# Kernel optimization log

Hardware: AMD Instinct MI355X
Metric: run time of the kernel (lower is better)

Reference implementation:

```python
import jax, jax.numpy as jnp
import numpy as np

TEMP = 0.05  # contrastive temperature (ContrastiveLoss.temp)
N, D = 8192, 128


def setup_inputs() -> dict:
    key = jax.random.key(0)
    k1, k2 = jax.random.split(key)
    x = jax.random.normal(k1, (N, D), dtype=jnp.float32)
    # Binary positive-pair label matrix; diagonal forced to 1 so every row
    # has at least one positive (positive_pair_nums > 0).
    y = (jax.random.uniform(k2, (N, N)) < 0.05).astype(jnp.float32)
    y = jnp.maximum(y, jnp.eye(N, dtype=jnp.float32))
    return {"x": x, "y": y}


def reference(x, y):
    # similarity(): L2-normalize rows, cosine matmul, exp(cos / temp)
    x_norm = x / jnp.linalg.norm(x, axis=1, keepdims=True)        # [N, D]
    cos_sim = jnp.exp(jnp.matmul(x_norm, x_norm.T) / TEMP)        # [N, N]

    positive_pair_nums = jnp.sum(y, axis=-1)                      # [N]
    neg_y = 1.0 - y
    # hard_mode == 'normal': negative mass per anchor
    nl = jnp.sum(cos_sim * neg_y, axis=-1, keepdims=True)         # [N, 1]

    # sm = log(cos_sim / (cos_sim + nl)); average over positives per row
    sm = jnp.log(cos_sim / (cos_sim + nl))                        # [N, N]
    lm = jnp.sum(sm * y, axis=-1) / positive_pair_nums            # [N]
    return -jnp.mean(lm)
```

## Files before the change

kernel.cpp:

```cpp
#include <hip/hip_runtime.h>
#include <hip/hip_bf16.h>


#define NN 8192

typedef short bf16x8 __attribute__((ext_vector_type(8)));
typedef float f32x4 __attribute__((ext_vector_type(4)));
typedef unsigned long long u64;
typedef unsigned int u32;

__device__ inline unsigned short f32_to_bf16_rne(float f) {
    unsigned u = __float_as_uint(f);
    unsigned r = 0x7FFFu + ((u >> 16) & 1u);
    return (unsigned short)((u + r) >> 16);
}

__global__ __launch_bounds__(256) void prep_kernel(
    const float* __restrict__ x, const float* __restrict__ y,
    unsigned short* __restrict__ xn, u64* __restrict__ bits) {
    const int t = threadIdx.x;
    const int w = t >> 6, l = t & 63;
    if (blockIdx.x < 2048) {
        const int row = blockIdx.x * 4 + w;
        float2 v = reinterpret_cast<const float2*>(x)[row * 64 + l];
        float ss = v.x * v.x + v.y * v.y;
#pragma unroll
        for (int m = 1; m < 64; m <<= 1) ss += __shfl_xor(ss, m);
        float rn = 1.0f / sqrtf(ss);
        ushort2 st;
        st.x = f32_to_bf16_rne(v.x * rn);
        st.y = f32_to_bf16_rne(v.y * rn);
        reinterpret_cast<ushort2*>(xn)[row * 64 + l] = st;
    } else {
        const int gw = (blockIdx.x - 2048) * 4 + w;
#pragma unroll 1
        for (int it = 0; it < 32; ++it) {
            const size_t w0 = ((size_t)it * 8192 + gw) * 4;
            u64 m0 = __ballot(y[(w0 + 0) * 64 + l] != 0.0f);
            u64 m1 = __ballot(y[(w0 + 1) * 64 + l] != 0.0f);
            u64 m2 = __ballot(y[(w0 + 2) * 64 + l] != 0.0f);
            u64 m3 = __ballot(y[(w0 + 3) * 64 + l] != 0.0f);
            if (l == 0) {
                bits[w0 + 0] = m0;
                bits[w0 + 1] = m1;
                bits[w0 + 2] = m2;
                bits[w0 + 3] = m3;
            }
        }
    }
}

template <bool DIAG>
__device__ __forceinline__ void epilogue(
    const f32x4 (&acc)[4][4], const u64 (&bw)[4], int l, int lm16, int lh4,
    int wM, int wN, int R0, int cb, float* __restrict__ Pt,
    float* __restrict__ sdg) {
#pragma unroll
    for (int qq = 0; qq < 4; ++qq) {
        float T = 0.0f, A = 0.0f, Y = 0.0f;
        const u32 lo = (u32)bw[qq];
        const u32 hi = (u32)(bw[qq] >> 32);
        const int rl = qq * 16 + lm16;
#pragma unroll
        for (int p = 0; p < 4; ++p) {
            const u32 wsel = (p < 2) ? lo : hi;
#pragma unroll
            for (int j = 0; j < 4; ++j) {
                float s = 20.0f * acc[p][qq][j];
                float e = __expf(s);
                float yv = (float)((wsel >> ((p & 1) * 16 + lh4 + j)) & 1u);
                if (DIAG) {
                    if (wM == wN && (p * 16 + lh4 + j) == rl) {
                        sdg[R0 + rl] = s;
                        e = 0.0f;
                        yv = 0.0f;
                    }
                }
                T += e;
                A = fmaf(yv, s, A);
                Y = fmaf(yv, e, Y);
            }
        }
        T += __shfl_xor(T, 16); T += __shfl_xor(T, 32);
        A += __shfl_xor(A, 16); A += __shfl_xor(A, 32);
        Y += __shfl_xor(Y, 16); Y += __shfl_xor(Y, 32);
        if (l < 16) {
            const size_t idx = (size_t)(cb * 2 + wM) * NN + (R0 + qq * 16 + l);
            Pt[idx] = T;
            Pt[1048576 + idx] = A;
            Pt[2 * 1048576 + idx] = Y;
        }
    }
}

__global__ __launch_bounds__(256, 3) void contrast_main_kernel(
    const unsigned short* __restrict__ xn, const u64* __restrict__ bits,
    float* __restrict__ Pt, float* __restrict__ sdg) {
    const int cb = blockIdx.x, rb = blockIdx.y;
    const int t = threadIdx.x;
    const int w = t >> 6, l = t & 63;
    const int wM = w >> 1, wN = w & 1;
    const int lm16 = l & 15, lh = l >> 4, lh4 = lh << 2;

    const int C0 = cb * 128 + wM * 64;
    const int R0 = rb * 128 + wN * 64;

    u64 bw[4];
#pragma unroll
    for (int qq = 0; qq < 4; ++qq)
        bw[qq] = bits[(size_t)(R0 + qq * 16 + lm16) * 128 + cb * 2 + wM];

    f32x4 acc[4][4];
#pragma unroll
    for (int i = 0; i < 4; ++i)
#pragma unroll
        for (int j = 0; j < 4; ++j) {
            f32x4 z = {0.0f, 0.0f, 0.0f, 0.0f};
            acc[i][j] = z;
        }

    const char* xb = reinterpret_cast<const char*>(xn);
#pragma unroll
    for (int ks = 0; ks < 4; ++ks) {
        bf16x8 af[4], bfr[4];
#pragma unroll
        for (int p = 0; p < 4; ++p) {
            const size_t c = (size_t)(C0 + p * 16 + lm16);
            af[p] = *reinterpret_cast<const bf16x8*>(xb + c * 256 + ks * 64 +
                                                     lh * 16);
        }
#pragma unroll
        for (int qq = 0; qq < 4; ++qq) {
            const size_t r = (size_t)(R0 + qq * 16 + lm16);
            bfr[qq] = *reinterpret_cast<const bf16x8*>(xb + r * 256 + ks * 64 +
                                                       lh * 16);
        }
#pragma unroll
        for (int p = 0; p < 4; ++p)
#pragma unroll
            for (int qq = 0; qq < 4; ++qq)
                acc[p][qq] = __builtin_amdgcn_mfma_f32_16x16x32_bf16(
                    af[p], bfr[qq], acc[p][qq], 0, 0, 0);
    }

    if (cb == rb)
        epilogue<true>(acc, bw, l, lm16, lh4, wM, wN, R0, cb, Pt, sdg);
    else
        epilogue<false>(acc, bw, l, lm16, lh4, wM, wN, R0, cb, Pt, sdg);
}

__global__ __launch_bounds__(256) void finalize_kernel(
    const float* __restrict__ Pt, const u64* __restrict__ bits,
    const float* __restrict__ sdg, float* __restrict__ out) {
    const int t = threadIdx.x;
    const int w = t >> 6, l = t & 63;
    const int r = blockIdx.x * 4 + w;

    const size_t base = (size_t)l * NN + r;
    float T = Pt[base] + Pt[base + (size_t)64 * NN];
    float A = Pt[1048576 + base] + Pt[1048576 + base + (size_t)64 * NN];
    float Y = Pt[2 * 1048576 + base] + Pt[2 * 1048576 + base + (size_t)64 * NN];
    u64 b0 = bits[(size_t)r * 128 + l];
    u64 b1 = bits[(size_t)r * 128 + 64 + l];
    float Pc = (float)(__popcll(b0) + __popcll(b1));
#pragma unroll
    for (int m = 1; m < 64; m <<= 1) {
        T += __shfl_xor(T, m);
        A += __shfl_xor(A, m);
        Y += __shfl_xor(Y, m);
        Pc += __shfl_xor(Pc, m);
    }

    __shared__ float red[4];
    if (l == 0) {
        const float nl = T - Y;
        const float sd = sdg[r];
        red[w] = (A - (Pc - 1.0f) * logf(nl) - log1pf(nl * __expf(-sd))) / Pc;
    }
    __syncthreads();
    if (t == 0) {
        float s = red[0] + red[1] + red[2] + red[3];
        atomicAdd(out, -s * (1.0f / (float)NN));
    }
}

extern "C" void kernel_launch(void* const* d_in, const int* in_sizes, int n_in,
                              void* d_out, int out_size, void* d_ws,
                              size_t ws_size, hipStream_t stream) {
    const float* x = (const float*)d_in[0];
    const float* y = (const float*)d_in[1];

    char* ws = (char*)d_ws;
    unsigned short* xn = (unsigned short*)ws;
    u64* bits = (u64*)(ws + (2ull << 20));
    float* Pt = (float*)(ws + (10ull << 20));
    float* sdg = (float*)(ws + (22ull << 20));

    hipMemsetAsync(d_out, 0, sizeof(float), stream);
    prep_kernel<<<4096, 256, 0, stream>>>(x, y, xn, bits);
    contrast_main_kernel<<<dim3(64, 64), 256, 0, stream>>>(xn, bits, Pt, sdg);
    finalize_kernel<<<NN / 4, 256, 0, stream>>>(Pt, bits, sdg, (float*)d_out);
}
```

Baseline: 473.6 us.

## Rewrite pipeline with LDS-staged tiles, row-major partials, vectorized bit packing

The y-to-bitmask pass now reads each row with float4 loads and packs four ballots per iteration, so a whole row goes through one wave. The main kernel moves to 512-thread blocks that stage both 128-row bf16 tiles into swizzled LDS via global_load_lds, with a block-index swizzle for L2 locality. Partials are stored row-major in three separate arrays so finalize reads contiguous float2 values. The atomic/memset final sum is replaced by a per-row loss buffer plus a single-block reduce kernel. This trades an extra launch and LDS occupancy limits for more coalesced traffic in the bandwidth-bound y pass and finalize.

```diff
diff --git a/kernel.cpp b/kernel.cpp
--- a/kernel.cpp
+++ b/kernel.cpp
@@ -32,19 +32,22 @@
         st.y = f32_to_bf16_rne(v.y * rn);
         reinterpret_cast<ushort2*>(xn)[row * 64 + l] = st;
     } else {
-        const int gw = (blockIdx.x - 2048) * 4 + w;
-#pragma unroll 1
-        for (int it = 0; it < 32; ++it) {
-            const size_t w0 = ((size_t)it * 8192 + gw) * 4;
-            u64 m0 = __ballot(y[(w0 + 0) * 64 + l] != 0.0f);
-            u64 m1 = __ballot(y[(w0 + 1) * 64 + l] != 0.0f);
-            u64 m2 = __ballot(y[(w0 + 2) * 64 + l] != 0.0f);
-            u64 m3 = __ballot(y[(w0 + 3) * 64 + l] != 0.0f);
+        const int r = (blockIdx.x - 2048) * 4 + w;
+        const float4* yr =
+            reinterpret_cast<const float4*>(y + (size_t)r * NN);
+        u64* br = bits + (size_t)r * 128;
+#pragma unroll 4
+        for (int g = 0; g < 32; ++g) {
+            float4 v = yr[g * 64 + l];
+            u64 m0 = __ballot(v.x != 0.0f);
+            u64 m1 = __ballot(v.y != 0.0f);
+            u64 m2 = __ballot(v.z != 0.0f);
+            u64 m3 = __ballot(v.w != 0.0f);
             if (l == 0) {
-                bits[w0 + 0] = m0;
-                bits[w0 + 1] = m1;
-                bits[w0 + 2] = m2;
-                bits[w0 + 3] = m3;
+                br[g * 4 + 0] = m0;
+                br[g * 4 + 1] = m1;
+                br[g * 4 + 2] = m2;
+                br[g * 4 + 3] = m3;
             }
         }
     }
@@ -52,136 +55,190 @@
 
 template <bool DIAG>
 __device__ __forceinline__ void epilogue(
-    const f32x4 (&acc)[4][4], const u64 (&bw)[4], int l, int lm16, int lh4,
-    int wM, int wN, int R0, int cb, float* __restrict__ Pt,
+    const f32x4 (&acc)[4][2], const u32 (&W0)[4], const u32 (&W1)[4],
+    int shbase, int wM, int wN, int lm16, int lh, int l, int rb, int cb,
+    float* __restrict__ PtT, float* __restrict__ PtA, float* __restrict__ PtY,
     float* __restrict__ sdg) {
 #pragma unroll
-    for (int qq = 0; qq < 4; ++qq) {
+    for (int qq = 0; qq < 2; ++qq) {
         float T = 0.0f, A = 0.0f, Y = 0.0f;
-        const u32 lo = (u32)bw[qq];
-        const u32 hi = (u32)(bw[qq] >> 32);
-        const int rl = qq * 16 + lm16;
+        const int rl = wN * 32 + qq * 16 + lm16;
 #pragma unroll
         for (int p = 0; p < 4; ++p) {
-            const u32 wsel = (p < 2) ? lo : hi;
+            const int cl = wM * 64 + p * 16 + lh * 4;
 #pragma unroll
             for (int j = 0; j < 4; ++j) {
                 float s = 20.0f * acc[p][qq][j];
                 float e = __expf(s);
-                float yv = (float)((wsel >> ((p & 1) * 16 + lh4 + j)) & 1u);
+                u32 word = qq ? W1[j] : W0[j];
+                u32 bit = (word >> (shbase + p * 4)) & 1u;
                 if (DIAG) {
-                    if (wM == wN && (p * 16 + lh4 + j) == rl) {
-                        sdg[R0 + rl] = s;
+                    if (cl + j == rl) {
+                        sdg[rb * 128 + rl] = s;
                         e = 0.0f;
-                        yv = 0.0f;
+                        bit = 0u;
                     }
                 }
                 T += e;
-                A = fmaf(yv, s, A);
-                Y = fmaf(yv, e, Y);
+                A += bit ? s : 0.0f;
+                Y += bit ? e : 0.0f;
             }
         }
         T += __shfl_xor(T, 16); T += __shfl_xor(T, 32);
         A += __shfl_xor(A, 16); A += __shfl_xor(A, 32);
         Y += __shfl_xor(Y, 16); Y += __shfl_xor(Y, 32);
         if (l < 16) {
-            const size_t idx = (size_t)(cb * 2 + wM) * NN + (R0 + qq * 16 + l);
-            Pt[idx] = T;
-            Pt[1048576 + idx] = A;
-            Pt[2 * 1048576 + idx] = Y;
-        }
-    }
-}
-
-__global__ __launch_bounds__(256, 3) void contrast_main_kernel(
+            const size_t idx =
+                (size_t)(rb * 128 + wN * 32 + qq * 16 + l) * 128 + cb * 2 + wM;
+            PtT[idx] = T;
+            PtA[idx] = A;
+            PtY[idx] = Y;
+        }
+    }
+}
+
+__global__ __launch_bounds__(512, 4) void contrast_main_kernel(
     const unsigned short* __restrict__ xn, const u64* __restrict__ bits,
-    float* __restrict__ Pt, float* __restrict__ sdg) {
-    const int cb = blockIdx.x, rb = blockIdx.y;
+    float* __restrict__ PtT, float* __restrict__ PtA, float* __restrict__ PtY,
+    float* __restrict__ sdg) {
+    __shared__ __align__(1024) char lds[65536];
+
+    const int bid = blockIdx.x;
+    const int swz = (bid & 7) * 512 + (bid >> 3);
+    const int cb = swz & 63, rb = swz >> 6;
     const int t = threadIdx.x;
     const int w = t >> 6, l = t & 63;
-    const int wM = w >> 1, wN = w & 1;
-    const int lm16 = l & 15, lh = l >> 4, lh4 = lh << 2;
-
-    const int C0 = cb * 128 + wM * 64;
-    const int R0 = rb * 128 + wN * 64;
-
-    u64 bw[4];
-#pragma unroll
-    for (int qq = 0; qq < 4; ++qq)
-        bw[qq] = bits[(size_t)(R0 + qq * 16 + lm16) * 128 + cb * 2 + wM];
-
-    f32x4 acc[4][4];
+    const int wM = w & 1, wN = w >> 1;
+    const int lm16 = l & 15, lh = l >> 4;
+
+    const int g4 = (cb >> 1) * 4;
+    const int rbase = rb * 128 + wN * 32;
+    u64 B0[4], B1[4];
+    {
+        const u64* bp0 = bits + (size_t)(rbase + lm16) * 128 + g4;
+        const u64* bp1 = bits + (size_t)(rbase + 16 + lm16) * 128 + g4;
+        ulonglong2 a0 = *reinterpret_cast<const ulonglong2*>(bp0);
+        ulonglong2 a1 = *reinterpret_cast<const ulonglong2*>(bp0 + 2);
+        ulonglong2 c0 = *reinterpret_cast<const ulonglong2*>(bp1);
+        ulonglong2 c1 = *reinterpret_cast<const ulonglong2*>(bp1 + 2);
+        B0[0] = a0.x; B0[1] = a0.y; B0[2] = a1.x; B0[3] = a1.y;
+        B1[0] = c0.x; B1[1] = c0.y; B1[2] = c1.x; B1[3] = c1.y;
+    }
+    const int base = (cb & 1) * 32 + wM * 16;
+    const bool hi = base >= 32;
+    u32 W0[4], W1[4];
+#pragma unroll
+    for (int e = 0; e < 4; ++e) {
+        W0[e] = hi ? (u32)(B0[e] >> 32) : (u32)B0[e];
+        W1[e] = hi ? (u32)(B1[e] >> 32) : (u32)B1[e];
+    }
+    const int shbase = (base & 31) + lh;
+
+    {
+        const char* xb = reinterpret_cast<const char*>(xn);
+        const char* srcA = xb + (size_t)cb * 32768;
+        const char* srcB = xb + (size_t)rb * 32768;
+#pragma unroll
+        for (int i = 0; i < 8; ++i) {
+            const int p = i * 8192 + t * 16;
+            const int pp = p & 32767;
+            const int src = pp ^ (((pp >> 8) & 7) << 4);
+            __builtin_amdgcn_global_load_lds(
+                (const __attribute__((address_space(1))) void*)(
+                    (i < 4 ? srcA : srcB) + src),
+                (__attribute__((address_space(3))) void*)(lds + p), 16, 0, 0);
+        }
+    }
+    asm volatile("s_waitcnt vmcnt(0)" ::: "memory");
+    __syncthreads();
+
+    f32x4 acc[4][2];
 #pragma unroll
     for (int i = 0; i < 4; ++i)
 #pragma unroll
-        for (int j = 0; j < 4; ++j) {
+        for (int j = 0; j < 2; ++j) {
             f32x4 z = {0.0f, 0.0f, 0.0f, 0.0f};
             acc[i][j] = z;
         }
 
-    const char* xb = reinterpret_cast<const char*>(xn);
 #pragma unroll
     for (int ks = 0; ks < 4; ++ks) {
-        bf16x8 af[4], bfr[4];
+        bf16x8 af[4], bfr[2];
 #pragma unroll
         for (int p = 0; p < 4; ++p) {
-            const size_t c = (size_t)(C0 + p * 16 + lm16);
-            af[p] = *reinterpret_cast<const bf16x8*>(xb + c * 256 + ks * 64 +
-                                                     lh * 16);
-        }
-#pragma unroll
-        for (int qq = 0; qq < 4; ++qq) {
-            const size_t r = (size_t)(R0 + qq * 16 + lm16);
-            bfr[qq] = *reinterpret_cast<const bf16x8*>(xb + r * 256 + ks * 64 +
-                                                       lh * 16);
+            const int c = wM * 64 + p * 16 + lm16;
+            const int v = c * 256 + ks * 64 + lh * 16;
+            af[p] = *reinterpret_cast<const bf16x8*>(lds + (v ^ ((c & 7) << 4)));
+        }
+#pragma unroll
+        for (int qq = 0; qq < 2; ++qq) {
+            const int r = wN * 32 + qq * 16 + lm16;
+            const int v = r * 256 + ks * 64 + lh * 16;
+            bfr[qq] = *reinterpret_cast<const bf16x8*>(
+                lds + 32768 + (v ^ ((r & 7) << 4)));
         }
 #pragma unroll
         for (int p = 0; p < 4; ++p)
 #pragma unroll
-            for (int qq = 0; qq < 4; ++qq)
+            for (int qq = 0; qq < 2; ++qq)
                 acc[p][qq] = __builtin_amdgcn_mfma_f32_16x16x32_bf16(
                     af[p], bfr[qq], acc[p][qq], 0, 0, 0);
     }
 
-    if (cb == rb)
-        epilogue<true>(acc, bw, l, lm16, lh4, wM, wN, R0, cb, Pt, sdg);
+    if (rb == cb)
+        epilogue<true>(acc, W0, W1, shbase, wM, wN, lm16, lh, l, rb, cb, PtT,
+                       PtA, PtY, sdg);
     else
-        epilogue<false>(acc, bw, l, lm16, lh4, wM, wN, R0, cb, Pt, sdg);
-}
-
-__global__ __launch_bounds__(256) void finalize_kernel(
-    const float* __restrict__ Pt, const u64* __restrict__ bits,
-    const float* __restrict__ sdg, float* __restrict__ out) {
+        epilogue<false>(acc, W0, W1, shbase, wM, wN, lm16, lh, l, rb, cb, PtT,
+                        PtA, PtY, sdg);
+}
+
+__global__ __launch_bounds__(1024) void finalize_kernel(
+    const float* __restrict__ PtT, const float* __restrict__ PtA,
+    const float* __restrict__ PtY, const u64* __restrict__ bits,
+    const float* __restrict__ sdg, float* __restrict__ rowloss) {
     const int t = threadIdx.x;
     const int w = t >> 6, l = t & 63;
-    const int r = blockIdx.x * 4 + w;
-
-    const size_t base = (size_t)l * NN + r;
-    float T = Pt[base] + Pt[base + (size_t)64 * NN];
-    float A = Pt[1048576 + base] + Pt[1048576 + base + (size_t)64 * NN];
-    float Y = Pt[2 * 1048576 + base] + Pt[2 * 1048576 + base + (size_t)64 * NN];
-    u64 b0 = bits[(size_t)r * 128 + l];
-    u64 b1 = bits[(size_t)r * 128 + 64 + l];
-    float Pc = (float)(__popcll(b0) + __popcll(b1));
+    const int r = blockIdx.x * 16 + w;
+
+    float2 vT = reinterpret_cast<const float2*>(PtT + (size_t)r * 128)[l];
+    float2 vA = reinterpret_cast<const float2*>(PtA + (size_t)r * 128)[l];
+    float2 vY = reinterpret_cast<const float2*>(PtY + (size_t)r * 128)[l];
+    ulonglong2 bb =
+        reinterpret_cast<const ulonglong2*>(bits + (size_t)r * 128)[l];
+    float T = vT.x + vT.y, A = vA.x + vA.y, Y = vY.x + vY.y;
+    float P = (float)(__popcll(bb.x) + __popcll(bb.y));
 #pragma unroll
     for (int m = 1; m < 64; m <<= 1) {
         T += __shfl_xor(T, m);
         A += __shfl_xor(A, m);
         Y += __shfl_xor(Y, m);
-        Pc += __shfl_xor(Pc, m);
-    }
-
-    __shared__ float red[4];
+        P += __shfl_xor(P, m);
+    }
     if (l == 0) {
         const float nl = T - Y;
-        const float sd = sdg[r];
-        red[w] = (A - (Pc - 1.0f) * logf(nl) - log1pf(nl * __expf(-sd))) / Pc;
-    }
+        rowloss[r] =
+            (A - (P - 1.0f) * logf(nl) - log1pf(nl * __expf(-sdg[r]))) / P;
+    }
+}
+
+__global__ void reduce_kernel(const float* __restrict__ rowloss,
+                              float* __restrict__ out) {
+    __shared__ float red[256];
+    const int t = threadIdx.x;
+    float s = 0.0f;
+#pragma unroll
+    for (int i = 0; i < 8; ++i) {
+        float4 v = reinterpret_cast<const float4*>(rowloss)[i * 256 + t];
+        s += v.x + v.y + v.z + v.w;
+    }
+    red[t] = s;
     __syncthreads();
-    if (t == 0) {
-        float s = red[0] + red[1] + red[2] + red[3];
-        atomicAdd(out, -s * (1.0f / (float)NN));
-    }
+    for (int k = 128; k > 0; k >>= 1) {
+        if (t < k) red[t] += red[t + k];
+        __syncthreads();
+    }
+    if (t == 0) out[0] = -red[0] / (float)NN;
 }
 
 extern "C" void kernel_launch(void* const* d_in, const int* in_sizes, int n_in,
@@ -193,11 +250,16 @@
     char* ws = (char*)d_ws;
     unsigned short* xn = (unsigned short*)ws;
     u64* bits = (u64*)(ws + (2ull << 20));
-    float* Pt = (float*)(ws + (10ull << 20));
+    float* PtT = (float*)(ws + (10ull << 20));
+    float* PtA = (float*)(ws + (14ull << 20));
+    float* PtY = (float*)(ws + (18ull << 20));
     float* sdg = (float*)(ws + (22ull << 20));
-
-    hipMemsetAsync(d_out, 0, sizeof(float), stream);
+    float* rowloss = (float*)(ws + (22ull << 20) + 32768);
+
     prep_kernel<<<4096, 256, 0, stream>>>(x, y, xn, bits);
-    contrast_main_kernel<<<dim3(64, 64), 256, 0, stream>>>(xn, bits, Pt, sdg);
-    finalize_kernel<<<NN / 4, 256, 0, stream>>>(Pt, bits, sdg, (float*)d_out);
-}
+    contrast_main_kernel<<<4096, 512, 0, stream>>>(xn, bits, PtT, PtA, PtY,
+                                                   sdg);
+    finalize_kernel<<<512, 1024, 0, stream>>>(PtT, PtA, PtY, bits, sdg,
+                                              rowloss);
+    reduce_kernel<<<1, 256, 0, stream>>>(rowloss, (float*)d_out);
+}
```

Result: faster. 411.4 us (-13.1%).
